# Optimization experiments

Measured on AMD Instinct MI355X. Metric: run time of the kernel, lower is better.

## Reference

```python
import jax, jax.numpy as jnp
import numpy as np
from jax import lax

T, H, I, E, K = 1024, 1024, 512, 16, 4


def setup_inputs() -> dict:
    key = jax.random.key(0)
    k1, k2, k3, k4, k5 = jax.random.split(key, 5)
    hidden_states = jax.random.normal(k1, (T, H), dtype=jnp.float32)
    top_k_index = jax.random.randint(k2, (T, K), 0, E)
    top_k_weights = jax.random.uniform(k3, (T, K), dtype=jnp.float32)
    gate_up_proj = jax.random.normal(k4, (E, 2 * I, H), dtype=jnp.float32) * 0.02
    down_proj = jax.random.normal(k5, (E, H, I), dtype=jnp.float32) * 0.02
    return {
        "hidden_states": hidden_states,
        "top_k_index": top_k_index,
        "top_k_weights": top_k_weights,
        "gate_up_proj": gate_up_proj,
        "down_proj": down_proj,
    }


def reference(hidden_states, top_k_index, top_k_weights, gate_up_proj, down_proj):
    num_experts = gate_up_proj.shape[0]
    # combine[t, e] = sum_k top_k_weights[t, k] * [top_k_index[t, k] == e]
    # Expert output is linear in the routing weight, so summing weights over
    # duplicate (token, expert) hits matches the original index_add_ exactly.
    one_hot = jax.nn.one_hot(top_k_index, num_experts, dtype=hidden_states.dtype)  # [T, K, E]
    combine = jnp.einsum("tke,tk->te", one_hot, top_k_weights)  # [T, E]

    def expert_step(acc, xs):
        w_gu, w_d, c = xs  # [2I, H], [H, I], [T]
        gu = hidden_states @ w_gu.T          # [T, 2I]
        gate, up = jnp.split(gu, 2, axis=-1)
        h = jax.nn.silu(gate) * up            # [T, I]
        out = h @ w_d.T                       # [T, H]
        return acc + out * c[:, None], None

    final, _ = lax.scan(
        expert_step,
        jnp.zeros_like(hidden_states),
        (gate_up_proj, down_proj, combine.T),
    )
    return final
```

## Files before the change

kernel.cpp:

```cpp
#include <hip/hip_runtime.h>
#include <hip/hip_bf16.h>
#include <cstdint>
#include <cstddef>

#define T_TOK 1024
#define HDIM  1024
#define IDIM  512
#define NEXP  16
#define TOPK  4
#define CAP   1024
#define GROUP 3

typedef __bf16 bf16;
typedef __attribute__((ext_vector_type(8))) __bf16 bf16x8;
typedef __attribute__((ext_vector_type(4))) __bf16 bf16x4;
typedef __attribute__((ext_vector_type(4))) float f32x4;

__device__ __forceinline__ void lds_load16(void* lds_dst, const void* g_src) {
  __builtin_amdgcn_global_load_lds(
      (__attribute__((address_space(1))) unsigned int*)(void*)(g_src),
      (__attribute__((address_space(3))) unsigned int*)(lds_dst),
      16, 0, 0);
}

__device__ __forceinline__ bf16x4 cvt4(float4 a) {
  bf16x4 o;
  o[0] = (bf16)a.x; o[1] = (bf16)a.y; o[2] = (bf16)a.z; o[3] = (bf16)a.w;
  return o;
}


#define CVT_BLOCKS (T_TOK * HDIM / 4 / 256)

__global__ void prep_kernel(const float* __restrict__ hid_f, bf16* __restrict__ hid_b,
                            const int* __restrict__ idx, const float* __restrict__ w,
                            int* __restrict__ etk, float* __restrict__ ew,
                            int* __restrict__ cntpad) {
  __shared__ int cnt;
  const int b = blockIdx.x;
  const int tid = threadIdx.x;
  if (b < CVT_BLOCKS) {
    int i = b * 256 + tid;
    float4 v = ((const float4*)hid_f)[i];
    ((bf16x4*)hid_b)[i] = cvt4(v);
    if (b == 0)
      ((bf16x4*)(hid_b + (size_t)T_TOK * HDIM))[tid] = cvt4(make_float4(0.f, 0.f, 0.f, 0.f));
    return;
  }
  const int e = b - CVT_BLOCKS;
  if (tid == 0) cnt = 0;
  __syncthreads();
  for (int j = tid; j < T_TOK * TOPK; j += blockDim.x) {
    if (idx[j] == e) {
      int slot = atomicAdd(&cnt, 1);
      if (slot < CAP) { etk[e * CAP + slot] = j; ew[e * CAP + slot] = w[j]; }
    }
  }
  __syncthreads();
  int c = cnt < CAP ? cnt : CAP;
  int p = (c + 63) & ~63;
  for (int j = c + tid; j < p; j += blockDim.x) {
    etk[e * CAP + j] = (T_TOK << 2);
    ew[e * CAP + j] = 0.f;
  }
  if (tid == 0) cntpad[e] = p;
}


__global__ __launch_bounds__(256, 4) void gemm1_kernel(
    const bf16* __restrict__ hid,
    const float* __restrict__ gup,
    const int* __restrict__ etk, const float* __restrict__ ew,
    const int* __restrict__ cntpad,
    bf16* __restrict__ hsc) {
  __shared__ __align__(16) bf16 As[GROUP][64 * 64];
  __shared__ __align__(16) bf16 BgS[16 * 64];
  __shared__ __align__(16) bf16 BuS[16 * 64];
  const int e  = blockIdx.y;
  const int z  = blockIdx.z;
  const int trips = cntpad[e] >> 6;
  const int n0 = blockIdx.x * 16;
  const int ebase = e * CAP;
  const int tid = threadIdx.x, lane = tid & 63, wid = tid >> 6;
  const int wm = wid * 16;
  const int lcol = lane & 15, lquad = lane >> 4;
  const int srow = tid >> 3;
  const int swz  = ((tid & 7) ^ (srow & 7)) * 8;
  const int br = tid >> 4;
  const int bc = (tid & 15) * 4;
  const int wb = (((bc >> 3) ^ (br & 7)) * 8) + (bc & 7);
  const float* gBg = gup + (size_t)e * (2 * IDIM) * HDIM + (size_t)(n0 + br) * HDIM + bc;
  const float* gBu = gBg + (size_t)IDIM * HDIM;

  for (int mg = z; mg < trips; mg += 2 * GROUP) {
    int tg = (trips - mg + 1) >> 1;
    if (tg > GROUP) tg = GROUP;
    const bf16 *gA0[GROUP], *gA1[GROUP];
#pragma unroll
    for (int mt = 0; mt < GROUP; ++mt)
      if (mt < tg) {
        const int mb = ebase + (mg + 2 * mt) * 64;
        gA0[mt] = hid + (size_t)(etk[mb + srow] >> 2) * HDIM + swz;
        gA1[mt] = hid + (size_t)(etk[mb + srow + 32] >> 2) * HDIM + swz;
      }
    f32x4 aG[GROUP], aU[GROUP];
#pragma unroll
    for (int mt = 0; mt < GROUP; ++mt) {
      aG[mt] = f32x4{0.f, 0.f, 0.f, 0.f};
      aU[mt] = f32x4{0.f, 0.f, 0.f, 0.f};
    }
    for (int k = 0; k < HDIM / 64; ++k) {
      float4 vg = *(const float4*)(gBg + k * 64);
      float4 vu = *(const float4*)(gBu + k * 64);
      __syncthreads();
#pragma unroll
      for (int mt = 0; mt < GROUP; ++mt)
        if (mt < tg) {
          lds_load16(&As[mt][tid * 8],        gA0[mt] + k * 64);
          lds_load16(&As[mt][tid * 8 + 2048], gA1[mt] + k * 64);
        }
      *(bf16x4*)&BgS[br * 64 + wb] = cvt4(vg);
      *(bf16x4*)&BuS[br * 64 + wb] = cvt4(vu);
      __syncthreads();
#pragma unroll
      for (int ks = 0; ks < 2; ++ks) {
        const int lch = ks * 4 + lquad;
        bf16x8 bg = *(const bf16x8*)&BgS[lcol * 64 + ((lch ^ (lcol & 7)) * 8)];
        bf16x8 bu = *(const bf16x8*)&BuS[lcol * 64 + ((lch ^ (lcol & 7)) * 8)];
        const int ar = wm + lcol;
        const int aoff = ar * 64 + ((lch ^ (ar & 7)) * 8);
#pragma unroll
        for (int mt = 0; mt < GROUP; ++mt)
          if (mt < tg) {
            bf16x8 af = *(const bf16x8*)&As[mt][aoff];
            aG[mt] = __builtin_amdgcn_mfma_f32_16x16x32_bf16(af, bg, aG[mt], 0, 0, 0);
            aU[mt] = __builtin_amdgcn_mfma_f32_16x16x32_bf16(af, bu, aU[mt], 0, 0, 0);
          }
      }
    }
#pragma unroll
    for (int mt = 0; mt < GROUP; ++mt)
      if (mt < tg) {
#pragma unroll
        for (int rr = 0; rr < 4; ++rr) {
          const int erow = (mg + 2 * mt) * 64 + wm + lquad * 4 + rr;
          const float wgt = ew[ebase + erow];
          float g = aG[mt][rr], u = aU[mt][rr];
          float s = g / (1.f + __expf(-g));
          hsc[(size_t)(ebase + erow) * IDIM + n0 + lcol] = (bf16)(s * u * wgt);
        }
      }
  }
}


__global__ __launch_bounds__(256, 4) void gemm2_kernel(
    const bf16* __restrict__ hsc,
    const float* __restrict__ down,
    const int* __restrict__ etk, const int* __restrict__ cntpad,
    float* __restrict__ slabs) {
  __shared__ __align__(16) bf16 As[GROUP][64 * 64];
  __shared__ __align__(16) bf16 Bs[16 * 64];
  const int e  = blockIdx.y;
  const int z  = blockIdx.z;
  const int trips = cntpad[e] >> 6;
  const int n0 = blockIdx.x * 16;
  const int ebase = e * CAP;
  const int tid = threadIdx.x, lane = tid & 63, wid = tid >> 6;
  const int wm = wid * 16;
  const int lcol = lane & 15, lquad = lane >> 4;
  const int srow = tid >> 3;
  const int swz  = ((tid & 7) ^ (srow & 7)) * 8;
  const int br = tid >> 4;
  const int bc = (tid & 15) * 4;
  const int wb = (((bc >> 3) ^ (br & 7)) * 8) + (bc & 7);
  const float* gB = down + (size_t)e * HDIM * IDIM + (size_t)(n0 + br) * IDIM + bc;

  for (int mg = z; mg < trips; mg += 2 * GROUP) {
    int tg = (trips - mg + 1) >> 1;
    if (tg > GROUP) tg = GROUP;
    const bf16 *gA0[GROUP], *gA1[GROUP];
#pragma unroll
    for (int mt = 0; mt < GROUP; ++mt)
      if (mt < tg) {
        const size_t rbase = (size_t)(ebase + (mg + 2 * mt) * 64);
        gA0[mt] = hsc + (rbase + srow) * IDIM + swz;
        gA1[mt] = hsc + (rbase + srow + 32) * IDIM + swz;
      }
    f32x4 acc[GROUP];
#pragma unroll
    for (int mt = 0; mt < GROUP; ++mt) acc[mt] = f32x4{0.f, 0.f, 0.f, 0.f};

    for (int k = 0; k < IDIM / 64; ++k) {
      float4 vb = *(const float4*)(gB + k * 64);
      __syncthreads();
#pragma unroll
      for (int mt = 0; mt < GROUP; ++mt)
        if (mt < tg) {
          lds_load16(&As[mt][tid * 8],        gA0[mt] + k * 64);
          lds_load16(&As[mt][tid * 8 + 2048], gA1[mt] + k * 64);
        }
      *(bf16x4*)&Bs[br * 64 + wb] = cvt4(vb);
      __syncthreads();
#pragma unroll
      for (int ks = 0; ks < 2; ++ks) {
        const int lch = ks * 4 + lquad;
        bf16x8 bv = *(const bf16x8*)&Bs[lcol * 64 + ((lch ^ (lcol & 7)) * 8)];
        const int ar = wm + lcol;
        const int aoff = ar * 64 + ((lch ^ (ar & 7)) * 8);
#pragma unroll
        for (int mt = 0; mt < GROUP; ++mt)
          if (mt < tg) {
            bf16x8 af = *(const bf16x8*)&As[mt][aoff];
            acc[mt] = __builtin_amdgcn_mfma_f32_16x16x32_bf16(af, bv, acc[mt], 0, 0, 0);
          }
      }
    }
#pragma unroll
    for (int mt = 0; mt < GROUP; ++mt)
      if (mt < tg) {
#pragma unroll
        for (int rr = 0; rr < 4; ++rr) {
          const int tk = etk[ebase + (mg + 2 * mt) * 64 + wm + lquad * 4 + rr];
          const int tok = tk >> 2, kslot = tk & 3;
          slabs[((size_t)kslot * (T_TOK + 1) + tok) * HDIM + n0 + lcol] = acc[mt][rr];
        }
      }
  }
}


__global__ void reduce_kernel(const float* __restrict__ slabs, float* __restrict__ out) {
  const size_t stride = (size_t)(T_TOK + 1) * HDIM;
  int i = blockIdx.x * blockDim.x + threadIdx.x;
  float4 a = ((const float4*)slabs)[i];
  float4 b = ((const float4*)(slabs + stride))[i];
  float4 c = ((const float4*)(slabs + 2 * stride))[i];
  float4 d = ((const float4*)(slabs + 3 * stride))[i];
  float4 o;
  o.x = a.x + b.x + c.x + d.x;
  o.y = a.y + b.y + c.y + d.y;
  o.z = a.z + b.z + c.z + d.z;
  o.w = a.w + b.w + c.w + d.w;
  ((float4*)out)[i] = o;
}


extern "C" void kernel_launch(void* const* d_in, const int* in_sizes, int n_in,
                              void* d_out, int out_size, void* d_ws, size_t ws_size,
                              hipStream_t stream) {
  const float* hid_f  = (const float*)d_in[0];
  const int*   idx    = (const int*)d_in[1];
  const float* tw     = (const float*)d_in[2];
  const float* gup_f  = (const float*)d_in[3];
  const float* down_f = (const float*)d_in[4];
  float* out = (float*)d_out;

  uint8_t* ws = (uint8_t*)d_ws;
  size_t off = 0;
  bf16* hid_b = (bf16*)(ws + off);   off += (size_t)(T_TOK + 1) * HDIM * 2;
  int*  etk   = (int*)(ws + off);    off += (size_t)NEXP * CAP * 4;
  float* ewt  = (float*)(ws + off);  off += (size_t)NEXP * CAP * 4;
  int* cntpad = (int*)(ws + off);    off += 256;
  bf16* hsc   = (bf16*)(ws + off);   off += (size_t)NEXP * CAP * IDIM * 2;
  float* slabs = (float*)(ws + off);

  prep_kernel<<<dim3(CVT_BLOCKS + NEXP), dim3(256), 0, stream>>>(
      hid_f, hid_b, idx, tw, etk, ewt, cntpad);
  gemm1_kernel<<<dim3(IDIM / 16, NEXP, 2), dim3(256), 0, stream>>>(
      hid_b, gup_f, etk, ewt, cntpad, hsc);
  gemm2_kernel<<<dim3(HDIM / 16, NEXP, 2), dim3(256), 0, stream>>>(
      hsc, down_f, etk, cntpad, slabs);
  reduce_kernel<<<dim3(T_TOK * HDIM / 4 / 256), dim3(256), 0, stream>>>(slabs, out);
}
```

Before: 191.2 us.

## Retile expert GEMMs to 128-row tiles with double-buffered LDS pipelining

Both expert GEMM kernels are retiled. Each block now computes a 128-row M tile against a wider N slice (32 gate/up columns or 64 down columns), with four register fragments per wave. The K loop double-buffers the A and B tiles in shared memory so that global loads for the next step overlap the MFMAs on the current one, and the padding granularity becomes 128 rows. The aim is more MFMA work per loaded byte and fewer weight re-reads across blocks, at the cost of more LDS and registers (launch bound occupancy lowered to 3) and more padded rows per expert.

```diff
diff --git a/kernel.cpp b/kernel.cpp
--- a/kernel.cpp
+++ b/kernel.cpp
@@ -9,7 +9,6 @@
 #define NEXP  16
 #define TOPK  4
 #define CAP   1024
-#define GROUP 3
 
 typedef __bf16 bf16;
 typedef __attribute__((ext_vector_type(8))) __bf16 bf16x8;
@@ -58,7 +57,7 @@
   }
   __syncthreads();
   int c = cnt < CAP ? cnt : CAP;
-  int p = (c + 63) & ~63;
+  int p = (c + 127) & ~127;
   for (int j = c + tid; j < p; j += blockDim.x) {
     etk[e * CAP + j] = (T_TOK << 2);
     ew[e * CAP + j] = 0.f;
@@ -67,165 +66,203 @@
 }
 
 
-__global__ __launch_bounds__(256, 4) void gemm1_kernel(
+__global__ __launch_bounds__(256, 3) void gemm1_kernel(
     const bf16* __restrict__ hid,
     const float* __restrict__ gup,
     const int* __restrict__ etk, const float* __restrict__ ew,
     const int* __restrict__ cntpad,
     bf16* __restrict__ hsc) {
-  __shared__ __align__(16) bf16 As[GROUP][64 * 64];
-  __shared__ __align__(16) bf16 BgS[16 * 64];
-  __shared__ __align__(16) bf16 BuS[16 * 64];
-  const int e  = blockIdx.y;
-  const int z  = blockIdx.z;
-  const int trips = cntpad[e] >> 6;
-  const int n0 = blockIdx.x * 16;
+  __shared__ __align__(16) bf16 As[2][128 * 64];
+  __shared__ __align__(16) bf16 Bs[2][64 * 64];
+  const int e = blockIdx.y, z = blockIdx.z;
+  const int ntiles = cntpad[e] >> 7;
+  const int n0 = blockIdx.x * 32;
   const int ebase = e * CAP;
   const int tid = threadIdx.x, lane = tid & 63, wid = tid >> 6;
-  const int wm = wid * 16;
+  const int wm = (wid >> 1) * 64, wi = (wid & 1) * 16;
   const int lcol = lane & 15, lquad = lane >> 4;
+  const int l7 = lcol & 7;
   const int srow = tid >> 3;
-  const int swz  = ((tid & 7) ^ (srow & 7)) * 8;
-  const int br = tid >> 4;
-  const int bc = (tid & 15) * 4;
-  const int wb = (((bc >> 3) ^ (br & 7)) * 8) + (bc & 7);
-  const float* gBg = gup + (size_t)e * (2 * IDIM) * HDIM + (size_t)(n0 + br) * HDIM + bc;
-  const float* gBu = gBg + (size_t)IDIM * HDIM;
-
-  for (int mg = z; mg < trips; mg += 2 * GROUP) {
-    int tg = (trips - mg + 1) >> 1;
-    if (tg > GROUP) tg = GROUP;
-    const bf16 *gA0[GROUP], *gA1[GROUP];
-#pragma unroll
-    for (int mt = 0; mt < GROUP; ++mt)
-      if (mt < tg) {
-        const int mb = ebase + (mg + 2 * mt) * 64;
-        gA0[mt] = hid + (size_t)(etk[mb + srow] >> 2) * HDIM + swz;
-        gA1[mt] = hid + (size_t)(etk[mb + srow + 32] >> 2) * HDIM + swz;
-      }
-    f32x4 aG[GROUP], aU[GROUP];
-#pragma unroll
-    for (int mt = 0; mt < GROUP; ++mt) {
-      aG[mt] = f32x4{0.f, 0.f, 0.f, 0.f};
-      aU[mt] = f32x4{0.f, 0.f, 0.f, 0.f};
-    }
-    for (int k = 0; k < HDIM / 64; ++k) {
-      float4 vg = *(const float4*)(gBg + k * 64);
-      float4 vu = *(const float4*)(gBu + k * 64);
-      __syncthreads();
-#pragma unroll
-      for (int mt = 0; mt < GROUP; ++mt)
-        if (mt < tg) {
-          lds_load16(&As[mt][tid * 8],        gA0[mt] + k * 64);
-          lds_load16(&As[mt][tid * 8 + 2048], gA1[mt] + k * 64);
-        }
-      *(bf16x4*)&BgS[br * 64 + wb] = cvt4(vg);
-      *(bf16x4*)&BuS[br * 64 + wb] = cvt4(vu);
-      __syncthreads();
+  const int swz = ((tid & 7) ^ (srow & 7)) * 8;
+  const int r = tid >> 2;
+  const int c0 = (tid & 3) * 4;
+  const int grow = (r < 32) ? (n0 + r) : (IDIM + n0 + (r - 32));
+  const float* gB = gup + (size_t)e * (2 * IDIM) * HDIM + (size_t)grow * HDIM + c0;
+  int wb[4];
+#pragma unroll
+  for (int j = 0; j < 4; ++j) {
+    int c = c0 + 16 * j;
+    wb[j] = (((c >> 3) ^ (r & 7)) * 8) + (c & 7);
+  }
+  const int bst = r * 64;
+
+  for (int mt = z; mt < ntiles; mt += 3) {
+    const int mrow = ebase + mt * 128;
+    const bf16* gA[4];
+#pragma unroll
+    for (int q = 0; q < 4; ++q)
+      gA[q] = hid + (size_t)(etk[mrow + srow + 32 * q] >> 2) * HDIM + swz;
+    f32x4 aG[4], aU[4];
+#pragma unroll
+    for (int mf = 0; mf < 4; ++mf) {
+      aG[mf] = f32x4{0.f, 0.f, 0.f, 0.f};
+      aU[mf] = f32x4{0.f, 0.f, 0.f, 0.f};
+    }
+    {
+      float4 bv[4];
+#pragma unroll
+      for (int j = 0; j < 4; ++j) bv[j] = *(const float4*)(gB + 16 * j);
+#pragma unroll
+      for (int q = 0; q < 4; ++q)
+        lds_load16(&As[0][tid * 8 + q * 2048], gA[q]);
+#pragma unroll
+      for (int j = 0; j < 4; ++j)
+        *(bf16x4*)&Bs[0][bst + wb[j]] = cvt4(bv[j]);
+    }
+    __syncthreads();
+#pragma unroll 2
+    for (int k = 0; k < 16; ++k) {
+      const int cur = k & 1, nxt = cur ^ 1;
+      float4 bn[4];
+      if (k < 15) {
+#pragma unroll
+        for (int q = 0; q < 4; ++q)
+          lds_load16(&As[nxt][tid * 8 + q * 2048], gA[q] + (k + 1) * 64);
+#pragma unroll
+        for (int j = 0; j < 4; ++j)
+          bn[j] = *(const float4*)(gB + (k + 1) * 64 + 16 * j);
+      }
 #pragma unroll
       for (int ks = 0; ks < 2; ++ks) {
         const int lch = ks * 4 + lquad;
-        bf16x8 bg = *(const bf16x8*)&BgS[lcol * 64 + ((lch ^ (lcol & 7)) * 8)];
-        bf16x8 bu = *(const bf16x8*)&BuS[lcol * 64 + ((lch ^ (lcol & 7)) * 8)];
-        const int ar = wm + lcol;
-        const int aoff = ar * 64 + ((lch ^ (ar & 7)) * 8);
-#pragma unroll
-        for (int mt = 0; mt < GROUP; ++mt)
-          if (mt < tg) {
-            bf16x8 af = *(const bf16x8*)&As[mt][aoff];
-            aG[mt] = __builtin_amdgcn_mfma_f32_16x16x32_bf16(af, bg, aG[mt], 0, 0, 0);
-            aU[mt] = __builtin_amdgcn_mfma_f32_16x16x32_bf16(af, bu, aU[mt], 0, 0, 0);
-          }
-      }
-    }
-#pragma unroll
-    for (int mt = 0; mt < GROUP; ++mt)
-      if (mt < tg) {
-#pragma unroll
-        for (int rr = 0; rr < 4; ++rr) {
-          const int erow = (mg + 2 * mt) * 64 + wm + lquad * 4 + rr;
-          const float wgt = ew[ebase + erow];
-          float g = aG[mt][rr], u = aU[mt][rr];
-          float s = g / (1.f + __expf(-g));
-          hsc[(size_t)(ebase + erow) * IDIM + n0 + lcol] = (bf16)(s * u * wgt);
+        const int sw = (lch ^ l7) * 8;
+        bf16x8 bg = *(const bf16x8*)&Bs[cur][(wi + lcol) * 64 + sw];
+        bf16x8 bu = *(const bf16x8*)&Bs[cur][(32 + wi + lcol) * 64 + sw];
+#pragma unroll
+        for (int mf = 0; mf < 4; ++mf) {
+          bf16x8 af = *(const bf16x8*)&As[cur][(wm + mf * 16 + lcol) * 64 + sw];
+          aG[mf] = __builtin_amdgcn_mfma_f32_16x16x32_bf16(af, bg, aG[mf], 0, 0, 0);
+          aU[mf] = __builtin_amdgcn_mfma_f32_16x16x32_bf16(af, bu, aU[mf], 0, 0, 0);
         }
       }
-  }
-}
-
-
-__global__ __launch_bounds__(256, 4) void gemm2_kernel(
+      if (k < 15) {
+#pragma unroll
+        for (int j = 0; j < 4; ++j)
+          *(bf16x4*)&Bs[nxt][bst + wb[j]] = cvt4(bn[j]);
+      }
+      __syncthreads();
+    }
+#pragma unroll
+    for (int mf = 0; mf < 4; ++mf) {
+#pragma unroll
+      for (int rr = 0; rr < 4; ++rr) {
+        const int erow = mt * 128 + wm + mf * 16 + lquad * 4 + rr;
+        const float wgt = ew[ebase + erow];
+        float g = aG[mf][rr], u = aU[mf][rr];
+        float s = g / (1.f + __expf(-g));
+        hsc[(size_t)(ebase + erow) * IDIM + n0 + wi + lcol] = (bf16)(s * u * wgt);
+      }
+    }
+  }
+}
+
+
+__global__ __launch_bounds__(256, 3) void gemm2_kernel(
     const bf16* __restrict__ hsc,
     const float* __restrict__ down,
     const int* __restrict__ etk, const int* __restrict__ cntpad,
     float* __restrict__ slabs) {
-  __shared__ __align__(16) bf16 As[GROUP][64 * 64];
-  __shared__ __align__(16) bf16 Bs[16 * 64];
-  const int e  = blockIdx.y;
-  const int z  = blockIdx.z;
-  const int trips = cntpad[e] >> 6;
-  const int n0 = blockIdx.x * 16;
+  __shared__ __align__(16) bf16 As[2][128 * 64];
+  __shared__ __align__(16) bf16 Bs[2][64 * 64];
+  const int e = blockIdx.y, z = blockIdx.z;
+  const int ntiles = cntpad[e] >> 7;
+  const int n0 = blockIdx.x * 64;
   const int ebase = e * CAP;
   const int tid = threadIdx.x, lane = tid & 63, wid = tid >> 6;
-  const int wm = wid * 16;
+  const int wm = (wid >> 1) * 64, wh = (wid & 1) * 32;
   const int lcol = lane & 15, lquad = lane >> 4;
+  const int l7 = lcol & 7;
   const int srow = tid >> 3;
-  const int swz  = ((tid & 7) ^ (srow & 7)) * 8;
-  const int br = tid >> 4;
-  const int bc = (tid & 15) * 4;
-  const int wb = (((bc >> 3) ^ (br & 7)) * 8) + (bc & 7);
-  const float* gB = down + (size_t)e * HDIM * IDIM + (size_t)(n0 + br) * IDIM + bc;
-
-  for (int mg = z; mg < trips; mg += 2 * GROUP) {
-    int tg = (trips - mg + 1) >> 1;
-    if (tg > GROUP) tg = GROUP;
-    const bf16 *gA0[GROUP], *gA1[GROUP];
-#pragma unroll
-    for (int mt = 0; mt < GROUP; ++mt)
-      if (mt < tg) {
-        const size_t rbase = (size_t)(ebase + (mg + 2 * mt) * 64);
-        gA0[mt] = hsc + (rbase + srow) * IDIM + swz;
-        gA1[mt] = hsc + (rbase + srow + 32) * IDIM + swz;
-      }
-    f32x4 acc[GROUP];
-#pragma unroll
-    for (int mt = 0; mt < GROUP; ++mt) acc[mt] = f32x4{0.f, 0.f, 0.f, 0.f};
-
-    for (int k = 0; k < IDIM / 64; ++k) {
-      float4 vb = *(const float4*)(gB + k * 64);
-      __syncthreads();
-#pragma unroll
-      for (int mt = 0; mt < GROUP; ++mt)
-        if (mt < tg) {
-          lds_load16(&As[mt][tid * 8],        gA0[mt] + k * 64);
-          lds_load16(&As[mt][tid * 8 + 2048], gA1[mt] + k * 64);
-        }
-      *(bf16x4*)&Bs[br * 64 + wb] = cvt4(vb);
-      __syncthreads();
+  const int swz = ((tid & 7) ^ (srow & 7)) * 8;
+  const int r = tid >> 2;
+  const int c0 = (tid & 3) * 4;
+  const float* gB = down + (size_t)e * HDIM * IDIM + (size_t)(n0 + r) * IDIM + c0;
+  int wb[4];
+#pragma unroll
+  for (int j = 0; j < 4; ++j) {
+    int c = c0 + 16 * j;
+    wb[j] = (((c >> 3) ^ (r & 7)) * 8) + (c & 7);
+  }
+  const int bst = r * 64;
+
+  for (int mt = z; mt < ntiles; mt += 3) {
+    const size_t rbase = (size_t)(ebase + mt * 128);
+    const bf16* gA[4];
+#pragma unroll
+    for (int q = 0; q < 4; ++q)
+      gA[q] = hsc + (rbase + srow + 32 * q) * IDIM + swz;
+    f32x4 acc[4][2];
+#pragma unroll
+    for (int mf = 0; mf < 4; ++mf) {
+      acc[mf][0] = f32x4{0.f, 0.f, 0.f, 0.f};
+      acc[mf][1] = f32x4{0.f, 0.f, 0.f, 0.f};
+    }
+    {
+      float4 bv[4];
+#pragma unroll
+      for (int j = 0; j < 4; ++j) bv[j] = *(const float4*)(gB + 16 * j);
+#pragma unroll
+      for (int q = 0; q < 4; ++q)
+        lds_load16(&As[0][tid * 8 + q * 2048], gA[q]);
+#pragma unroll
+      for (int j = 0; j < 4; ++j)
+        *(bf16x4*)&Bs[0][bst + wb[j]] = cvt4(bv[j]);
+    }
+    __syncthreads();
+#pragma unroll 2
+    for (int k = 0; k < 8; ++k) {
+      const int cur = k & 1, nxt = cur ^ 1;
+      float4 bn[4];
+      if (k < 7) {
+#pragma unroll
+        for (int q = 0; q < 4; ++q)
+          lds_load16(&As[nxt][tid * 8 + q * 2048], gA[q] + (k + 1) * 64);
+#pragma unroll
+        for (int j = 0; j < 4; ++j)
+          bn[j] = *(const float4*)(gB + (k + 1) * 64 + 16 * j);
+      }
 #pragma unroll
       for (int ks = 0; ks < 2; ++ks) {
         const int lch = ks * 4 + lquad;
-        bf16x8 bv = *(const bf16x8*)&Bs[lcol * 64 + ((lch ^ (lcol & 7)) * 8)];
-        const int ar = wm + lcol;
-        const int aoff = ar * 64 + ((lch ^ (ar & 7)) * 8);
-#pragma unroll
-        for (int mt = 0; mt < GROUP; ++mt)
-          if (mt < tg) {
-            bf16x8 af = *(const bf16x8*)&As[mt][aoff];
-            acc[mt] = __builtin_amdgcn_mfma_f32_16x16x32_bf16(af, bv, acc[mt], 0, 0, 0);
-          }
-      }
-    }
-#pragma unroll
-    for (int mt = 0; mt < GROUP; ++mt)
-      if (mt < tg) {
-#pragma unroll
-        for (int rr = 0; rr < 4; ++rr) {
-          const int tk = etk[ebase + (mg + 2 * mt) * 64 + wm + lquad * 4 + rr];
-          const int tok = tk >> 2, kslot = tk & 3;
-          slabs[((size_t)kslot * (T_TOK + 1) + tok) * HDIM + n0 + lcol] = acc[mt][rr];
+        const int sw = (lch ^ l7) * 8;
+        bf16x8 b0 = *(const bf16x8*)&Bs[cur][(wh + lcol) * 64 + sw];
+        bf16x8 b1 = *(const bf16x8*)&Bs[cur][(wh + 16 + lcol) * 64 + sw];
+#pragma unroll
+        for (int mf = 0; mf < 4; ++mf) {
+          bf16x8 af = *(const bf16x8*)&As[cur][(wm + mf * 16 + lcol) * 64 + sw];
+          acc[mf][0] = __builtin_amdgcn_mfma_f32_16x16x32_bf16(af, b0, acc[mf][0], 0, 0, 0);
+          acc[mf][1] = __builtin_amdgcn_mfma_f32_16x16x32_bf16(af, b1, acc[mf][1], 0, 0, 0);
         }
       }
+      if (k < 7) {
+#pragma unroll
+        for (int j = 0; j < 4; ++j)
+          *(bf16x4*)&Bs[nxt][bst + wb[j]] = cvt4(bn[j]);
+      }
+      __syncthreads();
+    }
+#pragma unroll
+    for (int mf = 0; mf < 4; ++mf) {
+#pragma unroll
+      for (int rr = 0; rr < 4; ++rr) {
+        const int row = mt * 128 + wm + mf * 16 + lquad * 4 + rr;
+        const int tk = etk[ebase + row];
+        const int tok = tk >> 2, ksl = tk & 3;
+        float* orow = slabs + ((size_t)ksl * (T_TOK + 1) + tok) * HDIM + n0 + wh + lcol;
+        orow[0] = acc[mf][0][rr];
+        orow[16] = acc[mf][1][rr];
+      }
+    }
   }
 }
 
@@ -267,9 +304,9 @@
 
   prep_kernel<<<dim3(CVT_BLOCKS + NEXP), dim3(256), 0, stream>>>(
       hid_f, hid_b, idx, tw, etk, ewt, cntpad);
-  gemm1_kernel<<<dim3(IDIM / 16, NEXP, 2), dim3(256), 0, stream>>>(
+  gemm1_kernel<<<dim3(IDIM / 32, NEXP, 3), dim3(256), 0, stream>>>(
       hid_b, gup_f, etk, ewt, cntpad, hsc);
-  gemm2_kernel<<<dim3(HDIM / 16, NEXP, 2), dim3(256), 0, stream>>>(
+  gemm2_kernel<<<dim3(HDIM / 64, NEXP, 3), dim3(256), 0, stream>>>(
       hsc, down_f, etk, cntpad, slabs);
   reduce_kernel<<<dim3(T_TOK * HDIM / 4 / 256), dim3(256), 0, stream>>>(slabs, out);
 }
```

Result: faster. 172.5 us (-9.8%).
